# Optimization experiments

Hardware: AMD Instinct MI355X
Metric: run time of the kernel (lower is better)

The kernel has to match this reference:

```python
import jax, jax.numpy as jnp
import numpy as np

THRESHOLD = 0.15  # init kwarg


def setup_inputs() -> dict:
    key = jax.random.key(0)
    B, T, N = 64, 1024, 512
    inputs = jax.random.normal(key, (B, T, N), dtype=jnp.float32)
    return {"inputs": inputs}


def reference(inputs) -> jnp.ndarray:
    # inputs: [B, T, N]; Pearson correlation across the sample (time) axis.
    B, T, N = inputs.shape
    xc = inputs - jnp.mean(inputs, axis=1, keepdims=True)        # [B,T,N]
    cov = jnp.einsum('bti,btj->bij', xc, xc)                     # [B,N,N] (unnormalized; norm cancels)
    d = jnp.sqrt(jnp.diagonal(cov, axis1=1, axis2=2))            # [B,N]
    corr = cov / (d[:, :, None] * d[:, None, :])                 # [B,N,N]

    # Original loop: for i<j, if |corr[:,i,j]|>thr: mask = mask * one_hot(i).
    # Equivalent closed form: let fired[b,i] = any_{j>i} |corr[b,i,j]|>thr.
    #   0 fired rows -> all-ones mask
    #   1 fired row  -> one_hot of that i (repeated onehot(i) multiplies are idempotent)
    #   >=2 distinct fired rows -> onehot(i1)*onehot(i2)=0 -> all-zeros mask
    upper = jnp.triu(jnp.ones((N, N), dtype=bool), k=1)
    cond = (jnp.abs(corr) > THRESHOLD) & upper                   # [B,N,N]
    fired = jnp.any(cond, axis=2)                                # [B,N]
    num_fired = jnp.sum(fired, axis=1)                           # [B]

    ones = jnp.ones((B, N), dtype=jnp.float32)
    mask = jnp.where((num_fired == 0)[:, None], ones,
                     jnp.where((num_fired == 1)[:, None],
                               fired.astype(jnp.float32),
                               jnp.zeros_like(ones)))
    return mask
```

## Files before the change

### kernel.cpp

```cpp
#include <hip/hip_runtime.h>
#include <hip/hip_bf16.h>

#define BB 64
#define TT 1024
#define NN 512
#define LISTCAP (1u << 18)

static constexpr float THR = 0.15f;
static constexpr float SQ    = 6.0f / 127.0f;
static constexpr float INVSQ = 127.0f / 6.0f;

typedef __attribute__((ext_vector_type(4))) int i32x4;

__device__ __forceinline__ void gload16(const void* g, void* lds_dst) {
    __builtin_amdgcn_global_load_lds(
        (const __attribute__((address_space(1))) unsigned int*)g,
        (__attribute__((address_space(3))) unsigned int*)lds_dst, 16, 0, 0);
}

__global__ __launch_bounds__(512) void transpose_colsum(
    const float* __restrict__ x, char* __restrict__ xq,
    float* __restrict__ s1, float* __restrict__ dv,
    float* __restrict__ nh, float* __restrict__ nl,
    unsigned* __restrict__ fired, unsigned* __restrict__ cnt) {
    __shared__ float red[4][8][64];
    int b = blockIdx.x, ng = blockIdx.y;
    int n0 = ng * 64;
    int tid = threadIdx.x, w = tid >> 6, l = tid & 63;
    const float* xb = x + (size_t)b * TT * NN + n0 + l;
    float a1 = 0.f, a2 = 0.f, al = 0.f;
    int aq = 0;
    if (b == 0 && ng == 0 && tid == 64) *cnt = 0;

    char* pbase = xq + ((size_t)(b * 8 + ng) * 16) * 4096
                  + (unsigned)l * 64u
                  + ((((unsigned)(w >> 1)) ^ (((unsigned)l >> 1) & 3u)) << 4)
                  + (unsigned)(w & 1) * 8u;

    for (int tc = 0; tc < 2; ++tc) {
        #pragma unroll
        for (int i = 0; i < 8; ++i) {
            int t0 = tc * 512 + i * 64 + w * 8;
            unsigned lo = 0, hi = 0;
            #pragma unroll
            for (int j = 0; j < 8; ++j) {
                float v = xb[(size_t)(t0 + j) * NN];
                a1 += v;
                a2 += v * v;
                int q = __float2int_rn(v * INVSQ);
                q = q > 127 ? 127 : (q < -127 ? -127 : q);
                aq += q * q;
                float lr = fmaf((float)q, -SQ, v);
                al += lr * lr;
                unsigned byte = (unsigned)(q & 255);
                if (j < 4) lo |= byte << (8 * j);
                else       hi |= byte << (8 * (j - 4));
            }
            *(uint2*)(pbase + (size_t)(t0 >> 6) * 4096) = make_uint2(lo, hi);
        }
    }
    red[0][w][l] = a1; red[1][w][l] = a2; red[2][w][l] = (float)aq; red[3][w][l] = al;
    __syncthreads();
    if (tid < 64) {
        float r1 = 0.f, r2 = 0.f, rq = 0.f, rl = 0.f;
        #pragma unroll
        for (int k = 0; k < 8; ++k) {
            r1 += red[0][k][tid]; r2 += red[1][k][tid];
            rq += red[2][k][tid]; rl += red[3][k][tid];
        }
        size_t o = (size_t)b * NN + n0 + tid;
        s1[o] = r1;
        dv[o] = r2 - r1 * r1 * (1.0f / TT);
        nh[o] = SQ * sqrtf(rq);
        nl[o] = sqrtf(rl);
        fired[o] = 0u;
    }
}

__global__ __launch_bounds__(256, 8) void corr_mfma(
    const char* __restrict__ xq, const float* __restrict__ s1,
    const float* __restrict__ dv, const float* __restrict__ nh,
    const float* __restrict__ nl, unsigned* __restrict__ fired,
    unsigned* __restrict__ cnt, unsigned* __restrict__ list) {
    __shared__ uint4 ldsbuf[1024];
    char* base = (char*)ldsbuf;

    int id = blockIdx.x;
    int swz = ((id & 7) * 288) + (id >> 3);
    int b = swz / 36;
    int u = swz % 36;
    int ti = 0, rem = u;
    while (rem >= (8 - ti)) { rem -= (8 - ti); ++ti; }
    int tj = ti + rem;
    int i0 = ti * 64, j0 = tj * 64;
    bool diag = (ti == tj);

    int tid = threadIdx.x;
    int wave = tid >> 6, lane = tid & 63;
    int rl = lane & 15, kg = lane >> 4;

    const char* srcA = xq + ((size_t)(b * 8 + ti) * 16) * 4096 + tid * 16;
    const char* srcB = xq + ((size_t)(b * 8 + tj) * 16) * 4096 + tid * 16;

    auto STAGE = [&](int s, int buf) {
        char* d = base + (buf << 13) + wave * 1024;
        gload16(srcA + (size_t)s * 4096, d);
        if (!diag) gload16(srcB + (size_t)s * 4096, d + 4096);
    };

    int wr = wave >> 1, wc = wave & 1;
    bool skip_mm = diag && (wr == 1) && (wc == 0);

    unsigned aoff[2], boff[2];
    #pragma unroll
    for (int f = 0; f < 2; ++f) {
        unsigned ca = (unsigned)(32 * wr + 16 * f + rl);
        aoff[f] = ca * 64u + ((((unsigned)kg ^ ((ca >> 1) & 3u)) & 3u) << 4);
        unsigned cb2 = (unsigned)(32 * wc + 16 * f + rl);
        boff[f] = cb2 * 64u + ((((unsigned)kg ^ ((cb2 >> 1) & 3u)) & 3u) << 4);
    }
    unsigned bbase = diag ? 0u : 4096u;

    i32x4 acc[2][2];
    #pragma unroll
    for (int i = 0; i < 2; ++i)
        #pragma unroll
        for (int j = 0; j < 2; ++j)
            acc[i][j] = (i32x4)0;

    STAGE(0, 0);
    __syncthreads();

    for (int it = 0; it < 16; ++it) {
        if (it + 1 < 16) STAGE(it + 1, (it + 1) & 1);
        const char* cb = base + ((it & 1) << 13);
        if (!skip_mm) {
            i32x4 A[2], Bv[2];
            #pragma unroll
            for (int f = 0; f < 2; ++f) A[f] = *(const i32x4*)(cb + aoff[f]);
            #pragma unroll
            for (int f = 0; f < 2; ++f) Bv[f] = *(const i32x4*)(cb + bbase + boff[f]);
            #pragma unroll
            for (int fj = 0; fj < 2; ++fj)
                #pragma unroll
                for (int fi = 0; fi < 2; ++fi)
                    acc[fi][fj] = __builtin_amdgcn_mfma_i32_16x16x64_i8(
                        A[fi], Bv[fj], acc[fi][fj], 0, 0, 0);
        }
        __syncthreads();
    }

    const float thr2 = THR * THR;
    const float invT = 1.0f / TT;
    const float s2 = SQ * SQ;
    const float* s1b = s1 + (size_t)b * NN;
    const float* dvb = dv + (size_t)b * NN;
    const float* nhb = nh + (size_t)b * NN;
    const float* nlb = nl + (size_t)b * NN;
    unsigned* fb = fired + (size_t)b * NN;
    int rowb = i0 + 32 * wr + kg * 4;
    int colb = j0 + 32 * wc + rl;
    #pragma unroll
    for (int fj = 0; fj < 2; ++fj) {
        int gj = colb + 16 * fj;
        float sj = s1b[gj], djv = dvb[gj];
        float nhj = nhb[gj], nlj = nlb[gj];
        #pragma unroll
        for (int fi = 0; fi < 2; ++fi) {
            int gi0 = rowb + 16 * fi;
            #pragma unroll
            for (int r = 0; r < 4; ++r) {
                int gi = gi0 + r;
                if (gj > gi) {
                    float cc = s2 * (float)acc[fi][fj][r] - s1b[gi] * sj * invT;
                    float lim = thr2 * dvb[gi] * djv;
                    float nhi = nhb[gi], nli = nlb[gi];
                    float B = nli * nhj + nlj * nhi + nli * nlj
                              + 1e-3f * nhi * nhj;
                    float a = fabsf(cc);
                    float lo = a - B;
                    if (lo > 0.0f && lo * lo > lim) {
                        atomicOr(&fb[gi], 1u);
                    } else if ((a + B) * (a + B) > lim) {
                        unsigned idx = atomicAdd(cnt, 1u);
                        if (idx < LISTCAP)
                            list[idx] = ((unsigned)b << 18) | ((unsigned)gi << 9)
                                        | (unsigned)gj;
                    }
                }
            }
        }
    }
}

__global__ __launch_bounds__(256) void cleanup_pairs(
    const float* __restrict__ x, const float* __restrict__ s1,
    const float* __restrict__ dv, const unsigned* __restrict__ cnt,
    const unsigned* __restrict__ list, unsigned* __restrict__ fired) {
    unsigned n = *cnt;
    if (n > LISTCAP) n = LISTCAP;
    int lane = threadIdx.x & 63;
    int gw = (blockIdx.x * 256 + threadIdx.x) >> 6;
    int nw = (gridDim.x * 256) >> 6;
    for (unsigned p = gw; p < n; p += nw) {
        unsigned e = list[p];
        int b = e >> 18, i = (e >> 9) & 511, j = e & 511;
        const float* xb = x + (size_t)b * TT * NN;
        double s = 0.0;
        for (int t = lane; t < TT; t += 64)
            s += (double)xb[(size_t)t * NN + i] * (double)xb[(size_t)t * NN + j];
        #pragma unroll
        for (int o = 32; o > 0; o >>= 1)
            s += __shfl_xor(s, o, 64);
        if (lane == 0) {
            double cov = s - (double)s1[(size_t)b * NN + i]
                             * (double)s1[(size_t)b * NN + j] / (double)TT;
            double lim = (double)THR * (double)THR
                         * (double)dv[(size_t)b * NN + i]
                         * (double)dv[(size_t)b * NN + j];
            if (cov * cov > lim) atomicOr(&fired[(size_t)b * NN + i], 1u);
        }
    }
}

__global__ __launch_bounds__(512) void finalize_mask(
    const unsigned* __restrict__ fired, float* __restrict__ out) {
    int b = blockIdx.x;
    int n = threadIdx.x;
    unsigned f = fired[(size_t)b * NN + n];
    __shared__ int wsum[8];
    unsigned long long m = __ballot(f != 0u);
    int lane = n & 63;
    int w = n >> 6;
    if (lane == 0) wsum[w] = __popcll(m);
    __syncthreads();
    int cnt = 0;
    #pragma unroll
    for (int i = 0; i < 8; ++i) cnt += wsum[i];
    float val = (cnt == 0) ? 1.0f : ((cnt == 1) ? (f ? 1.0f : 0.0f) : 0.0f);
    out[(size_t)b * NN + n] = val;
}

extern "C" void kernel_launch(void* const* d_in, const int* in_sizes, int n_in,
                              void* d_out, int out_size, void* d_ws, size_t ws_size,
                              hipStream_t stream) {
    const float* x = (const float*)d_in[0];
    float* out = (float*)d_out;

    char* xq = (char*)d_ws;
    float* s1 = (float*)(xq + (size_t)BB * NN * TT);
    float* dv = s1 + (size_t)BB * NN;
    float* nh = dv + (size_t)BB * NN;
    float* nl = nh + (size_t)BB * NN;
    unsigned* fired = (unsigned*)(nl + (size_t)BB * NN);
    unsigned* cnt   = fired + (size_t)BB * NN;
    unsigned* list  = cnt + 16;

    transpose_colsum<<<dim3(BB, 8), 512, 0, stream>>>(x, xq, s1, dv, nh, nl,
                                                      fired, cnt);
    corr_mfma<<<dim3(2304), 256, 0, stream>>>(xq, s1, dv, nh, nl, fired, cnt, list);
    cleanup_pairs<<<128, 256, 0, stream>>>(x, s1, dv, cnt, list, fired);
    finalize_mask<<<BB, 512, 0, stream>>>(fired, out);
}
```

Measured before the change: 103.9 us.

## Split transpose-quantize by time slabs with coalesced float4 loads and LDS staging

The first kernel now partitions work by time slab rather than column group. Each thread reads float4 rows coalesced, packs int8 values in registers, stages the swizzled 4 KB pages in LDS and writes them out as contiguous 16-byte stores. Column statistics become per-slab partial sums, reduced in a new small kernel. This targets the strided scalar global loads and 8-byte scattered stores of the old kernel, at the cost of an extra launch, a partial-sum buffer and 64 KB of LDS per block.

```diff
diff --git a/kernel.cpp b/kernel.cpp
--- a/kernel.cpp
+++ b/kernel.cpp
@@ -18,63 +18,110 @@
         (__attribute__((address_space(3))) unsigned int*)lds_dst, 16, 0, 0);
 }
 
-__global__ __launch_bounds__(512) void transpose_colsum(
-    const float* __restrict__ x, char* __restrict__ xq,
-    float* __restrict__ s1, float* __restrict__ dv,
+__global__ __launch_bounds__(512) void transpose_quant(
+    const float* __restrict__ x, char* __restrict__ xq, float* __restrict__ part) {
+    __shared__ uint4 pages[4096];
+    int b = blockIdx.x, ts = blockIdx.y;
+    int tid = threadIdx.x;
+    int r = tid >> 7, cq = tid & 127;
+
+    const float* xr = x + ((size_t)b * TT + 128 * ts + 32 * r) * NN + 4 * cq;
+
+    float fa1[4] = {0.f, 0.f, 0.f, 0.f};
+    float fa2[4] = {0.f, 0.f, 0.f, 0.f};
+    float faq[4] = {0.f, 0.f, 0.f, 0.f};
+    float fal[4] = {0.f, 0.f, 0.f, 0.f};
+    unsigned pk[4][8];
+    #pragma unroll
+    for (int c = 0; c < 4; ++c)
+        #pragma unroll
+        for (int w = 0; w < 8; ++w) pk[c][w] = 0u;
+
+    #pragma unroll
+    for (int i = 0; i < 32; ++i) {
+        float4 v = *(const float4*)(xr + (size_t)i * NN);
+        #pragma unroll
+        for (int cc = 0; cc < 4; ++cc) {
+            float val = (cc == 0) ? v.x : (cc == 1) ? v.y : (cc == 2) ? v.z : v.w;
+            fa1[cc] += val;
+            fa2[cc] = fmaf(val, val, fa2[cc]);
+            int q = __float2int_rn(val * INVSQ);
+            q = q > 127 ? 127 : (q < -127 ? -127 : q);
+            float qf = (float)q;
+            faq[cc] = fmaf(qf, qf, faq[cc]);
+            float lr = fmaf(qf, -SQ, val);
+            fal[cc] = fmaf(lr, lr, fal[cc]);
+            pk[cc][i >> 2] |= ((unsigned)(q & 255)) << (8 * (i & 3));
+        }
+    }
+
+    int g = cq >> 4;
+    int sp = r >> 1;
+    char* pbase = (char*)pages + ((g << 1) + sp) * 4096;
+    unsigned mhi = ((unsigned)(r & 1)) << 1;
+    #pragma unroll
+    for (int w8 = 0; w8 < 8; ++w8) {
+        int cc = (w8 + cq) & 3;
+        int msub = (w8 >> 2) ^ ((cq >> 2) & 1);
+        unsigned cp = (unsigned)((4 * (cq & 15)) + cc);
+        unsigned slot = mhi + (unsigned)msub;
+        unsigned off = cp * 64u + (((slot ^ ((cp >> 1) & 3u)) & 3u) << 4);
+        *(uint4*)(pbase + off) = make_uint4(pk[cc][4 * msub], pk[cc][4 * msub + 1],
+                                            pk[cc][4 * msub + 2], pk[cc][4 * msub + 3]);
+    }
+
+    {
+        size_t pb = ((size_t)(b * 8 + ts) * 4 + r) * 128 + cq;
+        float4* p4 = (float4*)part;
+        size_t stride = (size_t)BB * 8 * 4 * 128;
+        p4[0 * stride + pb] = make_float4(fa1[0], fa1[1], fa1[2], fa1[3]);
+        p4[1 * stride + pb] = make_float4(fa2[0], fa2[1], fa2[2], fa2[3]);
+        p4[2 * stride + pb] = make_float4(faq[0], faq[1], faq[2], faq[3]);
+        p4[3 * stride + pb] = make_float4(fal[0], fal[1], fal[2], fal[3]);
+    }
+
+    __syncthreads();
+
+    int wv = tid >> 6, lane = tid & 63;
+    #pragma unroll
+    for (int pi = 0; pi < 2; ++pi) {
+        int p = 2 * wv + pi;
+        int pg = p >> 1, ps = p & 1;
+        const char* src = (const char*)pages + p * 4096 + lane * 16;
+        char* dst = xq + ((size_t)((b * 8 + pg) * 16) + 2 * ts + ps) * 4096 + lane * 16;
+        #pragma unroll
+        for (int it = 0; it < 4; ++it)
+            *(uint4*)(dst + (size_t)it * 1024) =
+                *(const uint4*)(src + (size_t)it * 1024);
+    }
+}
+
+__global__ __launch_bounds__(512) void colsum_reduce(
+    const float* __restrict__ part, float* __restrict__ s1, float* __restrict__ dv,
     float* __restrict__ nh, float* __restrict__ nl,
     unsigned* __restrict__ fired, unsigned* __restrict__ cnt) {
-    __shared__ float red[4][8][64];
-    int b = blockIdx.x, ng = blockIdx.y;
-    int n0 = ng * 64;
-    int tid = threadIdx.x, w = tid >> 6, l = tid & 63;
-    const float* xb = x + (size_t)b * TT * NN + n0 + l;
-    float a1 = 0.f, a2 = 0.f, al = 0.f;
-    int aq = 0;
-    if (b == 0 && ng == 0 && tid == 64) *cnt = 0;
-
-    char* pbase = xq + ((size_t)(b * 8 + ng) * 16) * 4096
-                  + (unsigned)l * 64u
-                  + ((((unsigned)(w >> 1)) ^ (((unsigned)l >> 1) & 3u)) << 4)
-                  + (unsigned)(w & 1) * 8u;
-
-    for (int tc = 0; tc < 2; ++tc) {
-        #pragma unroll
-        for (int i = 0; i < 8; ++i) {
-            int t0 = tc * 512 + i * 64 + w * 8;
-            unsigned lo = 0, hi = 0;
-            #pragma unroll
-            for (int j = 0; j < 8; ++j) {
-                float v = xb[(size_t)(t0 + j) * NN];
-                a1 += v;
-                a2 += v * v;
-                int q = __float2int_rn(v * INVSQ);
-                q = q > 127 ? 127 : (q < -127 ? -127 : q);
-                aq += q * q;
-                float lr = fmaf((float)q, -SQ, v);
-                al += lr * lr;
-                unsigned byte = (unsigned)(q & 255);
-                if (j < 4) lo |= byte << (8 * j);
-                else       hi |= byte << (8 * (j - 4));
-            }
-            *(uint2*)(pbase + (size_t)(t0 >> 6) * 4096) = make_uint2(lo, hi);
-        }
-    }
-    red[0][w][l] = a1; red[1][w][l] = a2; red[2][w][l] = (float)aq; red[3][w][l] = al;
-    __syncthreads();
-    if (tid < 64) {
-        float r1 = 0.f, r2 = 0.f, rq = 0.f, rl = 0.f;
-        #pragma unroll
-        for (int k = 0; k < 8; ++k) {
-            r1 += red[0][k][tid]; r2 += red[1][k][tid];
-            rq += red[2][k][tid]; rl += red[3][k][tid];
-        }
-        size_t o = (size_t)b * NN + n0 + tid;
-        s1[o] = r1;
-        dv[o] = r2 - r1 * r1 * (1.0f / TT);
-        nh[o] = SQ * sqrtf(rq);
-        nl[o] = sqrtf(rl);
-        fired[o] = 0u;
-    }
+    int b = blockIdx.x;
+    int c = threadIdx.x;
+    int cq = c >> 2, cc = c & 3;
+    size_t stride = (size_t)BB * 8 * 4 * 128 * 4;
+    float acc[4] = {0.f, 0.f, 0.f, 0.f};
+    #pragma unroll
+    for (int t4 = 0; t4 < 4; ++t4) {
+        float s = 0.f;
+        for (int sl = 0; sl < 32; ++sl) {
+            size_t idx = t4 * stride + (((size_t)(b * 8) + (sl >> 2)) * 4 + (sl & 3))
+                         * 512 + cq * 4 + cc;
+            s += part[idx];
+        }
+        acc[t4] = s;
+    }
+    size_t o = (size_t)b * NN + c;
+    s1[o] = acc[0];
+    dv[o] = acc[1] - acc[0] * acc[0] * (1.0f / TT);
+    nh[o] = SQ * sqrtf(acc[2]);
+    nl[o] = sqrtf(acc[3]);
+    fired[o] = 0u;
+    if (b == 0 && c == 0) *cnt = 0;
 }
 
 __global__ __launch_bounds__(256, 8) void corr_mfma(
@@ -248,7 +295,8 @@
     float* out = (float*)d_out;
 
     char* xq = (char*)d_ws;
-    float* s1 = (float*)(xq + (size_t)BB * NN * TT);
+    float* part = (float*)(xq + (size_t)BB * NN * TT);
+    float* s1 = part + (size_t)4 * BB * 8 * 4 * 512;
     float* dv = s1 + (size_t)BB * NN;
     float* nh = dv + (size_t)BB * NN;
     float* nl = nh + (size_t)BB * NN;
@@ -256,8 +304,8 @@
     unsigned* cnt   = fired + (size_t)BB * NN;
     unsigned* list  = cnt + 16;
 
-    transpose_colsum<<<dim3(BB, 8), 512, 0, stream>>>(x, xq, s1, dv, nh, nl,
-                                                      fired, cnt);
+    transpose_quant<<<dim3(BB, 8), 512, 0, stream>>>(x, xq, part);
+    colsum_reduce<<<BB, 512, 0, stream>>>(part, s1, dv, nh, nl, fired, cnt);
     corr_mfma<<<dim3(2304), 256, 0, stream>>>(xq, s1, dv, nh, nl, fired, cnt, list);
     cleanup_pairs<<<128, 256, 0, stream>>>(x, s1, dv, cnt, list, fired);
     finalize_mask<<<BB, 512, 0, stream>>>(fired, out);
```

After: 107.0 us. +2.9%, slower.

## Stage int8 transpose in LDS for coalesced stores and simplify error bound

Applied to the files above, without the earlier changes.

The quantize/transpose kernel now writes packed int8 values into an LDS tile first, then copies each 4KB chunk to global memory with 16-byte lane-contiguous stores. Before, each lane wrote scattered 8-byte pieces straight to global. The quantized-norm accumulator is dropped and replaced by the fp32 norm sqrt(sum v^2). The corr error bound uses this norm plus an extra 3x residual term, which may widen the bound and send more pairs to the cleanup list. This adds two block barriers per chunk and more LDS use.

```diff
diff --git a/kernel.cpp b/kernel.cpp
--- a/kernel.cpp
+++ b/kernel.cpp
@@ -21,21 +21,19 @@
 __global__ __launch_bounds__(512) void transpose_colsum(
     const float* __restrict__ x, char* __restrict__ xq,
     float* __restrict__ s1, float* __restrict__ dv,
-    float* __restrict__ nh, float* __restrict__ nl,
+    float* __restrict__ nv, float* __restrict__ nl,
     unsigned* __restrict__ fired, unsigned* __restrict__ cnt) {
-    __shared__ float red[4][8][64];
+    __shared__ uint4 tile[2048];
+    __shared__ float red[3][8][64];
     int b = blockIdx.x, ng = blockIdx.y;
     int n0 = ng * 64;
     int tid = threadIdx.x, w = tid >> 6, l = tid & 63;
     const float* xb = x + (size_t)b * TT * NN + n0 + l;
     float a1 = 0.f, a2 = 0.f, al = 0.f;
-    int aq = 0;
     if (b == 0 && ng == 0 && tid == 64) *cnt = 0;
 
-    char* pbase = xq + ((size_t)(b * 8 + ng) * 16) * 4096
-                  + (unsigned)l * 64u
-                  + ((((unsigned)(w >> 1)) ^ (((unsigned)l >> 1) & 3u)) << 4)
-                  + (unsigned)(w & 1) * 8u;
+    unsigned sw4 = ((((unsigned)w >> 1) ^ (((unsigned)l >> 1) & 3u)) & 3u);
+    unsigned wroff = (unsigned)l * 64u + (sw4 << 4) + ((unsigned)(w & 1)) * 8u;
 
     for (int tc = 0; tc < 2; ++tc) {
         #pragma unroll
@@ -46,32 +44,40 @@
             for (int j = 0; j < 8; ++j) {
                 float v = xb[(size_t)(t0 + j) * NN];
                 a1 += v;
-                a2 += v * v;
+                a2 = fmaf(v, v, a2);
                 int q = __float2int_rn(v * INVSQ);
                 q = q > 127 ? 127 : (q < -127 ? -127 : q);
-                aq += q * q;
                 float lr = fmaf((float)q, -SQ, v);
-                al += lr * lr;
+                al = fmaf(lr, lr, al);
                 unsigned byte = (unsigned)(q & 255);
                 if (j < 4) lo |= byte << (8 * j);
                 else       hi |= byte << (8 * (j - 4));
             }
-            *(uint2*)(pbase + (size_t)(t0 >> 6) * 4096) = make_uint2(lo, hi);
-        }
-    }
-    red[0][w][l] = a1; red[1][w][l] = a2; red[2][w][l] = (float)aq; red[3][w][l] = al;
+            *(uint2*)((char*)tile + i * 4096 + wroff) = make_uint2(lo, hi);
+        }
+        __syncthreads();
+        {
+            const char* src = (const char*)tile + w * 4096 + l * 16;
+            char* dst = xq + ((size_t)((b * 8 + ng) * 16) + tc * 8 + w) * 4096 + l * 16;
+            #pragma unroll
+            for (int it = 0; it < 4; ++it)
+                *(uint4*)(dst + (size_t)it * 1024) =
+                    *(const uint4*)(src + (size_t)it * 1024);
+        }
+        __syncthreads();
+    }
+    red[0][w][l] = a1; red[1][w][l] = a2; red[2][w][l] = al;
     __syncthreads();
     if (tid < 64) {
-        float r1 = 0.f, r2 = 0.f, rq = 0.f, rl = 0.f;
+        float r1 = 0.f, r2 = 0.f, rl = 0.f;
         #pragma unroll
         for (int k = 0; k < 8; ++k) {
-            r1 += red[0][k][tid]; r2 += red[1][k][tid];
-            rq += red[2][k][tid]; rl += red[3][k][tid];
+            r1 += red[0][k][tid]; r2 += red[1][k][tid]; rl += red[2][k][tid];
         }
         size_t o = (size_t)b * NN + n0 + tid;
         s1[o] = r1;
         dv[o] = r2 - r1 * r1 * (1.0f / TT);
-        nh[o] = SQ * sqrtf(rq);
+        nv[o] = sqrtf(r2);
         nl[o] = sqrtf(rl);
         fired[o] = 0u;
     }
@@ -79,7 +85,7 @@
 
 __global__ __launch_bounds__(256, 8) void corr_mfma(
     const char* __restrict__ xq, const float* __restrict__ s1,
-    const float* __restrict__ dv, const float* __restrict__ nh,
+    const float* __restrict__ dv, const float* __restrict__ nv,
     const float* __restrict__ nl, unsigned* __restrict__ fired,
     unsigned* __restrict__ cnt, unsigned* __restrict__ list) {
     __shared__ uint4 ldsbuf[1024];
@@ -155,7 +161,7 @@
     const float s2 = SQ * SQ;
     const float* s1b = s1 + (size_t)b * NN;
     const float* dvb = dv + (size_t)b * NN;
-    const float* nhb = nh + (size_t)b * NN;
+    const float* nvb = nv + (size_t)b * NN;
     const float* nlb = nl + (size_t)b * NN;
     unsigned* fb = fired + (size_t)b * NN;
     int rowb = i0 + 32 * wr + kg * 4;
@@ -164,7 +170,7 @@
     for (int fj = 0; fj < 2; ++fj) {
         int gj = colb + 16 * fj;
         float sj = s1b[gj], djv = dvb[gj];
-        float nhj = nhb[gj], nlj = nlb[gj];
+        float nvj = nvb[gj], nlj = nlb[gj];
         #pragma unroll
         for (int fi = 0; fi < 2; ++fi) {
             int gi0 = rowb + 16 * fi;
@@ -174,9 +180,9 @@
                 if (gj > gi) {
                     float cc = s2 * (float)acc[fi][fj][r] - s1b[gi] * sj * invT;
                     float lim = thr2 * dvb[gi] * djv;
-                    float nhi = nhb[gi], nli = nlb[gi];
-                    float B = nli * nhj + nlj * nhi + nli * nlj
-                              + 1e-3f * nhi * nhj;
+                    float nvi = nvb[gi], nli = nlb[gi];
+                    float B = nli * nvj + nlj * nvi + 3.0f * nli * nlj
+                              + 1e-3f * nvi * nvj;
                     float a = fabsf(cc);
                     float lo = a - B;
                     if (lo > 0.0f && lo * lo > lim) {
@@ -250,15 +256,15 @@
     char* xq = (char*)d_ws;
     float* s1 = (float*)(xq + (size_t)BB * NN * TT);
     float* dv = s1 + (size_t)BB * NN;
-    float* nh = dv + (size_t)BB * NN;
-    float* nl = nh + (size_t)BB * NN;
+    float* nv = dv + (size_t)BB * NN;
+    float* nl = nv + (size_t)BB * NN;
     unsigned* fired = (unsigned*)(nl + (size_t)BB * NN);
     unsigned* cnt   = fired + (size_t)BB * NN;
     unsigned* list  = cnt + 16;
 
-    transpose_colsum<<<dim3(BB, 8), 512, 0, stream>>>(x, xq, s1, dv, nh, nl,
+    transpose_colsum<<<dim3(BB, 8), 512, 0, stream>>>(x, xq, s1, dv, nv, nl,
                                                       fired, cnt);
-    corr_mfma<<<dim3(2304), 256, 0, stream>>>(xq, s1, dv, nh, nl, fired, cnt, list);
+    corr_mfma<<<dim3(2304), 256, 0, stream>>>(xq, s1, dv, nv, nl, fired, cnt, list);
     cleanup_pairs<<<128, 256, 0, stream>>>(x, s1, dv, cnt, list, fired);
     finalize_mask<<<BB, 512, 0, stream>>>(fired, out);
 }
```

New measurement: 92.15 us. 1.13x faster.
